# Performance work log

Hardware: AMD Instinct MI355X
Metric: run time of the kernel (lower is better)

## Reference

```python
import jax, jax.numpy as jnp
import numpy as np

N_HEAD = 16


def setup_inputs() -> dict:
    key = jax.random.key(0)
    ks = jax.random.split(key, 5)
    B, L, C = 2, 2048, 1024
    s = 0.02
    return {
        "x": jax.random.normal(ks[0], (B, L, C), dtype=jnp.float32),
        "attn_mask": jnp.ones((B, L), dtype=jnp.int64),
        "Wq": jax.random.normal(ks[1], (C, C), dtype=jnp.float32) * s,
        "Wk": jax.random.normal(ks[2], (C, C), dtype=jnp.float32) * s,
        "Wv": jax.random.normal(ks[3], (C, C), dtype=jnp.float32) * s,
        "Wp": jax.random.normal(ks[4], (C, C), dtype=jnp.float32) * s,
    }


def reference(x, attn_mask, Wq, Wk, Wv, Wp):
    B, L, C = x.shape
    H = N_HEAD
    D = C // H
    # nn.Linear(bias=False): y = x @ W.T with W of shape (out, in)
    q = (x @ Wq.T).reshape(B, L, H, D).transpose(0, 2, 1, 3)  # (B,H,L,D)
    k = (x @ Wk.T).reshape(B, L, H, D).transpose(0, 2, 1, 3)
    v = (x @ Wv.T).reshape(B, L, H, D).transpose(0, 2, 1, 3)
    att = jnp.einsum("bhqd,bhkd->bhqk", q, k) / jnp.sqrt(jnp.asarray(D, x.dtype))
    causal = jnp.tril(jnp.ones((L, L), dtype=bool))  # (L,L)
    tok = (attn_mask != 0)[:, None, None, :]  # (B,1,1,L) key-side padding mask
    mask = causal[None, None, :, :] & tok
    att = jnp.where(mask, att, -jnp.inf)
    att = jax.nn.softmax(att, axis=-1)
    # dropout p=0.0 (eval): identity
    y = jnp.einsum("bhqk,bhkd->bhqd", att, v)
    y = y.transpose(0, 2, 1, 3).reshape(B, L, C)
    return y @ Wp.T
```

## Files before the change

### kernel.cpp

```cpp
#include <hip/hip_runtime.h>
#include <hip/hip_bf16.h>
#include <cstdint>

typedef _Float16 f16;
typedef _Float16 f16x4 __attribute__((ext_vector_type(4)));
typedef _Float16 f16x8 __attribute__((ext_vector_type(8)));
typedef float f32x4 __attribute__((ext_vector_type(4)));

#define LNEG (-1e30f)
#define EXP2(x) __builtin_amdgcn_exp2f(x)

__device__ __forceinline__ f32x4 mfma16(f16x8 a, f16x8 b, f32x4 c){
    return __builtin_amdgcn_mfma_f32_16x16x32_f16(a, b, c, 0, 0, 0);
}

__global__ __launch_bounds__(256) void cvt5(
    const float* __restrict__ x,  const float* __restrict__ wq,
    const float* __restrict__ wk, const float* __restrict__ wv,
    const float* __restrict__ wp, f16* __restrict__ dst, int nx8)
{
    int i = blockIdx.x * blockDim.x + threadIdx.x;
    const float* src; int off;
    if (i < nx8){ src = x; off = i; }
    else {
        int j = i - nx8;
        int s = j >> 17;
        off = j & 131071;
        src = (s == 0) ? wq : (s == 1) ? wk : (s == 2) ? wv : wp;
    }
    const float4* p = (const float4*)src + (size_t)off * 2;
    float4 v0 = p[0], v1 = p[1];
    f16x8 o = { (f16)v0.x, (f16)v0.y, (f16)v0.z, (f16)v0.w,
                (f16)v1.x, (f16)v1.y, (f16)v1.z, (f16)v1.w };
    *(f16x8*)&dst[(size_t)i * 8] = o;
}

template<typename OutT>
__global__ __launch_bounds__(256) void gemm_xwt(
    const f16* __restrict__ A, const f16* __restrict__ W0, size_t wstride,
    OutT* __restrict__ out0, size_t ostride, f16* __restrict__ vtout,
    int M, int N, int K)
{
    const int tid  = threadIdx.x;
    const int lane = tid & 63;
    const int w    = tid >> 6;
    const int wr   = w >> 1, wc = w & 1;
    const int m0   = blockIdx.y * 128;
    const int n0   = blockIdx.x * 128;
    const f16* Wz  = W0 + wstride * blockIdx.z;
    OutT* out      = out0 + ostride * blockIdx.z;

    __shared__ f16 At[2][128 * 64];
    __shared__ f16 Bt[2][128 * 64];

    f32x4 acc[4][4] = {};
    f16x8 avr[4], bvr[4];

    int srow[4], scolb[4], sswz[4];
    #pragma unroll
    for (int j = 0; j < 4; ++j){
        int off  = (j * 256 + tid) * 16;
        srow[j]  = off >> 7;
        scolb[j] = off & 127;
        sswz[j]  = srow[j] * 128 + (scolb[j] ^ ((srow[j] & 7) << 4));
    }

    #pragma unroll
    for (int j = 0; j < 4; ++j){
        avr[j] = *(const f16x8*)&A [(size_t)(m0 + srow[j]) * K + (scolb[j] >> 1)];
        bvr[j] = *(const f16x8*)&Wz[(size_t)(n0 + srow[j]) * K + (scolb[j] >> 1)];
    }
    #pragma unroll
    for (int j = 0; j < 4; ++j){
        *(f16x8*)((char*)At[0] + sswz[j]) = avr[j];
        *(f16x8*)((char*)Bt[0] + sswz[j]) = bvr[j];
    }
    __syncthreads();

    const int NT = K >> 6;
    for (int t = 0; t < NT; ++t){
        const int cur = t & 1;
        const bool pre = (t + 1 < NT);
        if (pre){
            const int k0 = (t + 1) << 6;
            #pragma unroll
            for (int j = 0; j < 4; ++j){
                avr[j] = *(const f16x8*)&A [(size_t)(m0 + srow[j]) * K + k0 + (scolb[j] >> 1)];
                bvr[j] = *(const f16x8*)&Wz[(size_t)(n0 + srow[j]) * K + k0 + (scolb[j] >> 1)];
            }
        }
        #pragma unroll
        for (int kk = 0; kk < 2; ++kk){
            f16x8 af[4], bf[4];
            #pragma unroll
            for (int mf = 0; mf < 4; ++mf){
                int row = wr * 64 + mf * 16 + (lane & 15);
                int cb  = (kk * 64 + 16 * (lane >> 4)) ^ ((row & 7) << 4);
                af[mf] = *(const f16x8*)((const char*)At[cur] + row * 128 + cb);
            }
            #pragma unroll
            for (int nf = 0; nf < 4; ++nf){
                int row = wc * 64 + nf * 16 + (lane & 15);
                int cb  = (kk * 64 + 16 * (lane >> 4)) ^ ((row & 7) << 4);
                bf[nf] = *(const f16x8*)((const char*)Bt[cur] + row * 128 + cb);
            }
            #pragma unroll
            for (int mf = 0; mf < 4; ++mf)
                #pragma unroll
                for (int nf = 0; nf < 4; ++nf)
                    acc[mf][nf] = mfma16(af[mf], bf[nf], acc[mf][nf]);
        }
        if (pre){
            const int nb = cur ^ 1;
            #pragma unroll
            for (int j = 0; j < 4; ++j){
                *(f16x8*)((char*)At[nb] + sswz[j]) = avr[j];
                *(f16x8*)((char*)Bt[nb] + sswz[j]) = bvr[j];
            }
        }
        __syncthreads();
    }

    if (vtout != nullptr && blockIdx.z == 2){
        #pragma unroll
        for (int mf = 0; mf < 4; ++mf)
            #pragma unroll
            for (int nf = 0; nf < 4; ++nf){
                int row = m0 + wr * 64 + mf * 16 + 4 * (lane >> 4);
                int col = n0 + wc * 64 + nf * 16 + (lane & 15);
                int bb = row >> 11, ll = row & 2047;
                int bh = bb * 16 + (col >> 6), dd = col & 63;
                f16x4 o = { (f16)acc[mf][nf][0], (f16)acc[mf][nf][1],
                            (f16)acc[mf][nf][2], (f16)acc[mf][nf][3] };
                *(f16x4*)&vtout[((size_t)(bh * 64 + dd)) * 2048 + ll] = o;
            }
    } else {
        #pragma unroll
        for (int mf = 0; mf < 4; ++mf)
            #pragma unroll
            for (int nf = 0; nf < 4; ++nf)
                #pragma unroll
                for (int r = 0; r < 4; ++r){
                    int row = m0 + wr * 64 + mf * 16 + 4 * (lane >> 4) + r;
                    int col = n0 + wc * 64 + nf * 16 + (lane & 15);
                    out[(size_t)row * N + col] = (OutT)acc[mf][nf][r];
                }
    }
}

__global__ __launch_bounds__(256) void gemm_proj64(
    const f16* __restrict__ A, const f16* __restrict__ W,
    float* __restrict__ out, int M, int N, int K)
{
    const int tid  = threadIdx.x;
    const int lane = tid & 63;
    const int wc   = tid >> 6;
    const int g    = lane >> 4;
    const int qq   = lane & 15;
    const int m0   = blockIdx.y * 64;
    const int n0   = blockIdx.x * 128;

    __shared__ f16 At[2][64 * 64];
    __shared__ f16 Bt[2][128 * 64];

    f32x4 acc[4][2] = {};
    f16x8 avr[2], bvr[4];

    int arow[2], acol[2], aswz[2];
    #pragma unroll
    for (int j = 0; j < 2; ++j){
        int c  = j * 256 + tid;
        arow[j] = c >> 3; acol[j] = (c & 7) * 8;
        aswz[j] = arow[j] * 128 + (((c & 7) * 16) ^ ((arow[j] & 7) << 4));
    }
    int brow[4], bcol[4], bswz[4];
    #pragma unroll
    for (int j = 0; j < 4; ++j){
        int c  = j * 256 + tid;
        brow[j] = c >> 3; bcol[j] = (c & 7) * 8;
        bswz[j] = brow[j] * 128 + (((c & 7) * 16) ^ ((brow[j] & 7) << 4));
    }

    #pragma unroll
    for (int j = 0; j < 2; ++j) avr[j] = *(const f16x8*)&A[(size_t)(m0 + arow[j]) * K + acol[j]];
    #pragma unroll
    for (int j = 0; j < 4; ++j) bvr[j] = *(const f16x8*)&W[(size_t)(n0 + brow[j]) * K + bcol[j]];
    #pragma unroll
    for (int j = 0; j < 2; ++j) *(f16x8*)((char*)At[0] + aswz[j]) = avr[j];
    #pragma unroll
    for (int j = 0; j < 4; ++j) *(f16x8*)((char*)Bt[0] + bswz[j]) = bvr[j];
    __syncthreads();

    const int NT = K >> 6;
    for (int t = 0; t < NT; ++t){
        const int cur = t & 1;
        const bool pre = (t + 1 < NT);
        if (pre){
            const int k0 = (t + 1) << 6;
            #pragma unroll
            for (int j = 0; j < 2; ++j) avr[j] = *(const f16x8*)&A[(size_t)(m0 + arow[j]) * K + k0 + acol[j]];
            #pragma unroll
            for (int j = 0; j < 4; ++j) bvr[j] = *(const f16x8*)&W[(size_t)(n0 + brow[j]) * K + k0 + bcol[j]];
        }
        #pragma unroll
        for (int kk = 0; kk < 2; ++kk){
            f16x8 af[4], bf[2];
            #pragma unroll
            for (int mf = 0; mf < 4; ++mf){
                int row = mf * 16 + qq;
                int cb  = (kk * 64 + 16 * g) ^ ((row & 7) << 4);
                af[mf] = *(const f16x8*)((const char*)At[cur] + row * 128 + cb);
            }
            #pragma unroll
            for (int nf = 0; nf < 2; ++nf){
                int row = wc * 32 + nf * 16 + qq;
                int cb  = (kk * 64 + 16 * g) ^ ((row & 7) << 4);
                bf[nf] = *(const f16x8*)((const char*)Bt[cur] + row * 128 + cb);
            }
            #pragma unroll
            for (int mf = 0; mf < 4; ++mf)
                #pragma unroll
                for (int nf = 0; nf < 2; ++nf)
                    acc[mf][nf] = mfma16(af[mf], bf[nf], acc[mf][nf]);
        }
        if (pre){
            const int nb = cur ^ 1;
            #pragma unroll
            for (int j = 0; j < 2; ++j) *(f16x8*)((char*)At[nb] + aswz[j]) = avr[j];
            #pragma unroll
            for (int j = 0; j < 4; ++j) *(f16x8*)((char*)Bt[nb] + bswz[j]) = bvr[j];
        }
        __syncthreads();
    }
    #pragma unroll
    for (int mf = 0; mf < 4; ++mf)
        #pragma unroll
        for (int nf = 0; nf < 2; ++nf)
            #pragma unroll
            for (int r = 0; r < 4; ++r){
                int row = m0 + mf * 16 + 4 * g + r;
                int col = n0 + wc * 32 + nf * 16 + qq;
                out[(size_t)row * N + col] = acc[mf][nf][r];
            }
}

__global__ __launch_bounds__(256, 4) void attn_fused(
    const f16* __restrict__ q, const f16* __restrict__ k,
    const f16* __restrict__ vt, const int* __restrict__ amask,
    f16* __restrict__ y, float* __restrict__ pO, float* __restrict__ pML)
{
    const int tid  = threadIdx.x;
    const int lane = tid & 63;
    const int w    = tid >> 6;
    const int g    = lane >> 4;
    const int qq   = lane & 15;

    const int lin = blockIdx.x;
    const int bh  = lin & 31;
    const int grp = lin >> 5;
    int qt, ktLo, ktHi, part; bool fin;
    if (grp < 4)      { qt = 19 - grp;  ktLo = 0;  ktHi = qt + 1; fin = true;  part = 0; }
    else if (grp < 16){ qt = 16 + grp;  ktLo = 0;  ktHi = 16;     fin = false; part = 0; }
    else if (grp < 28){ qt = 47 - grp;  ktLo = 16; ktHi = qt + 1; fin = false; part = 1; }
    else              { qt = 43 - grp;  ktLo = 0;  ktHi = qt + 1; fin = true;  part = 0; }

    const int b = bh >> 4, h = bh & 15;
    const int q0w = qt * 64 + w * 16;

    __shared__ char sK[2][64 * 128];
    __shared__ char sV[2][64 * 128];
    __shared__ char sP[4][16 * 128];

    const int srow = (tid * 2) >> 3;
    const int sc8a = (tid * 2) & 7, sc8b = sc8a + 1;
    const int swka = (sc8a * 16) ^ ((srow & 7) << 4);
    const int swkb = (sc8b * 16) ^ ((srow & 7) << 4);
    const f16* kbase  = k  + ((size_t)b * 2048) * 1024 + h * 64;
    const f16* vtbase = vt + (size_t)bh * 64 * 2048;

    const f16 qscale = (f16)(0.125f * 1.44269504088896f);
    f16x8 aq[2];
    #pragma unroll
    for (int f = 0; f < 2; ++f){
        aq[f] = *(const f16x8*)&q[((size_t)(b * 2048 + q0w + qq)) * 1024 + h * 64 + f * 32 + 8 * g];
        #pragma unroll
        for (int j = 0; j < 8; ++j) aq[f][j] *= qscale;
    }

    f32x4 acc_o[4] = {};
    float m_ln = LNEG, l_ln = 0.f;

    char* pbase = sP[w] + qq * 128;
    const int swp = (qq & 7) << 4;

    {
        const int k0p = ktLo * 64;
        f16x8 ka  = *(const f16x8*)(kbase  + (size_t)(k0p + srow) * 1024 + sc8a * 8);
        f16x8 kb2 = *(const f16x8*)(kbase  + (size_t)(k0p + srow) * 1024 + sc8b * 8);
        f16x8 va  = *(const f16x8*)(vtbase + (size_t)srow * 2048 + k0p + sc8a * 8);
        f16x8 vb  = *(const f16x8*)(vtbase + (size_t)srow * 2048 + k0p + sc8b * 8);
        *(f16x8*)(sK[0] + srow * 128 + swka) = ka;
        *(f16x8*)(sK[0] + srow * 128 + swkb) = kb2;
        *(f16x8*)(sV[0] + srow * 128 + swka) = va;
        *(f16x8*)(sV[0] + srow * 128 + swkb) = vb;
    }
    __syncthreads();

    for (int kt = ktLo; kt < ktHi; ++kt){
        const int cur = (kt - ktLo) & 1;
        const int k0 = kt * 64;
        const bool pre = (kt + 1 < ktHi);

        f16x8 ka, kb2, va, vb;
        if (pre){
            const int nk0 = k0 + 64;
            ka  = *(const f16x8*)(kbase  + (size_t)(nk0 + srow) * 1024 + sc8a * 8);
            kb2 = *(const f16x8*)(kbase  + (size_t)(nk0 + srow) * 1024 + sc8b * 8);
            va  = *(const f16x8*)(vtbase + (size_t)srow * 2048 + nk0 + sc8a * 8);
            vb  = *(const f16x8*)(vtbase + (size_t)srow * 2048 + nk0 + sc8b * 8);
        }

        unsigned long long tokbits = __ballot(amask[b * 2048 + k0 + lane] != 0);
        const bool tokall = (tokbits == ~0ull);

        f32x4 acc_s[4] = {};
        #pragma unroll
        for (int kf = 0; kf < 4; ++kf){
            const int keyl = kf * 16 + qq;
            const char* kr = sK[cur] + keyl * 128;
            const int sw = (keyl & 7) << 4;
            #pragma unroll
            for (int f = 0; f < 2; ++f){
                f16x8 ak = *(const f16x8*)(kr + ((f * 64 + 16 * g) ^ sw));
                acc_s[kf] = mfma16(ak, aq[f], acc_s[kf]);
            }
        }

        const bool fullt = (k0 + 63 <= q0w) && tokall;
        float sv[16];
        #pragma unroll
        for (int kf = 0; kf < 4; ++kf)
            #pragma unroll
            for (int r = 0; r < 4; ++r){
                float s = acc_s[kf][r];
                if (!fullt){
                    const int keyl = kf * 16 + 4 * g + r;
                    const bool ok = (k0 + keyl <= q0w + qq) && ((tokbits >> keyl) & 1);
                    s = ok ? s : LNEG;
                }
                sv[kf * 4 + r] = s;
            }

        float tmax = sv[0];
        #pragma unroll
        for (int i = 1; i < 16; ++i) tmax = fmaxf(tmax, sv[i]);
        tmax = fmaxf(tmax, __shfl_xor(tmax, 16));
        tmax = fmaxf(tmax, __shfl_xor(tmax, 32));
        const bool skip = __all(tmax <= m_ln + 8.f);
        float alpha = 1.f;
        if (!skip){
            const float newm = fmaxf(m_ln, tmax);
            alpha = EXP2(m_ln - newm);
            m_ln = newm;
        }
        float rs = 0.f;
        #pragma unroll
        for (int i = 0; i < 16; ++i){ sv[i] = EXP2(sv[i] - m_ln); rs += sv[i]; }
        rs += __shfl_xor(rs, 16);
        rs += __shfl_xor(rs, 32);
        l_ln = l_ln * alpha + rs;
        if (!skip){
            #pragma unroll
            for (int r = 0; r < 4; ++r){
                const float ar = __shfl(alpha, 4 * g + r);
                #pragma unroll
                for (int nf = 0; nf < 4; ++nf) acc_o[nf][r] *= ar;
            }
        }

        #pragma unroll
        for (int kf = 0; kf < 4; ++kf){
            f16x4 pk = { (f16)sv[kf*4+0], (f16)sv[kf*4+1], (f16)sv[kf*4+2], (f16)sv[kf*4+3] };
            *(f16x4*)(pbase + ((kf * 32 + 8 * g) ^ swp)) = pk;
        }
        asm volatile("s_waitcnt lgkmcnt(0)" ::: "memory");
        __builtin_amdgcn_sched_barrier(0);

        #pragma unroll
        for (int f = 0; f < 2; ++f){
            f16x8 ap = *(const f16x8*)(pbase + ((f * 64 + 16 * g) ^ swp));
            #pragma unroll
            for (int nf = 0; nf < 4; ++nf){
                const int d = nf * 16 + qq;
                f16x8 bv = *(const f16x8*)(sV[cur] + d * 128 + ((f * 64 + 16 * g) ^ ((d & 7) << 4)));
                acc_o[nf] = mfma16(ap, bv, acc_o[nf]);
            }
        }

        if (pre){
            const int nb = cur ^ 1;
            *(f16x8*)(sK[nb] + srow * 128 + swka) = ka;
            *(f16x8*)(sK[nb] + srow * 128 + swkb) = kb2;
            *(f16x8*)(sV[nb] + srow * 128 + swka) = va;
            *(f16x8*)(sV[nb] + srow * 128 + swkb) = vb;
        }
        __syncthreads();
    }

    if (fin){
        const float invl = 1.f / l_ln;
        #pragma unroll
        for (int r = 0; r < 4; ++r){
            const float ir = __shfl(invl, 4 * g + r);
            const int row = q0w + 4 * g + r;
            #pragma unroll
            for (int nf = 0; nf < 4; ++nf)
                y[((size_t)(b * 2048 + row)) * 1024 + h * 64 + nf * 16 + qq] = (f16)(acc_o[nf][r] * ir);
        }
    } else {
        const int qi = qt - 20;
        const size_t base = (((size_t)part * 12 + qi) * 32 + bh) * 64;
        #pragma unroll
        for (int r = 0; r < 4; ++r){
            const int row_local = w * 16 + 4 * g + r;
            float* po = pO + (base + row_local) * 64;
            #pragma unroll
            for (int nf = 0; nf < 4; ++nf)
                po[nf * 16 + qq] = acc_o[nf][r];
        }
        if (lane < 16){
            const size_t mlb = (base + w * 16 + lane) * 2;
            pML[mlb]     = m_ln;
            pML[mlb + 1] = l_ln;
        }
    }
}

__global__ __launch_bounds__(256) void attn_merge(
    const float* __restrict__ pO, const float* __restrict__ pML, f16* __restrict__ y)
{
    const int t = blockIdx.x * 256 + threadIdx.x;
    const int dc = (t & 3) * 16;
    const int rowg = t >> 2;
    const int row = rowg & 63;
    const int bh  = (rowg >> 6) & 31;
    const int qi  = rowg >> 11;
    const size_t rbase = ((size_t)qi * 32 + bh) * 64 + row;
    const size_t PST = (size_t)12 * 32 * 64;

    const float mA = pML[rbase * 2],         lA = pML[rbase * 2 + 1];
    const float mB = pML[(PST + rbase) * 2], lB = pML[(PST + rbase) * 2 + 1];
    const float m  = fmaxf(mA, mB);
    const float wA = EXP2(mA - m), wB = EXP2(mB - m);
    const float inv = 1.f / (wA * lA + wB * lB);

    const float4* oA = (const float4*)(pO + rbase * 64 + dc);
    const float4* oB = (const float4*)(pO + (PST * 64) + rbase * 64 + dc);
    float ov[16];
    #pragma unroll
    for (int j = 0; j < 4; ++j){
        float4 a = oA[j], bb4 = oB[j];
        ov[j*4+0] = (wA * a.x + wB * bb4.x) * inv;
        ov[j*4+1] = (wA * a.y + wB * bb4.y) * inv;
        ov[j*4+2] = (wA * a.z + wB * bb4.z) * inv;
        ov[j*4+3] = (wA * a.w + wB * bb4.w) * inv;
    }
    const int b = bh >> 4, h = bh & 15;
    const int grow = (20 + qi) * 64 + row;
    f16* yp = &y[((size_t)(b * 2048 + grow)) * 1024 + h * 64 + dc];
    f16x8 o0 = { (f16)ov[0],(f16)ov[1],(f16)ov[2],(f16)ov[3],(f16)ov[4],(f16)ov[5],(f16)ov[6],(f16)ov[7] };
    f16x8 o1 = { (f16)ov[8],(f16)ov[9],(f16)ov[10],(f16)ov[11],(f16)ov[12],(f16)ov[13],(f16)ov[14],(f16)ov[15] };
    *(f16x8*)yp = o0;
    *(f16x8*)(yp + 8) = o1;
}

extern "C" void kernel_launch(void* const* d_in, const int* in_sizes, int n_in,
                              void* d_out, int out_size, void* d_ws, size_t ws_size,
                              hipStream_t stream){
    const float* x  = (const float*)d_in[0];
    const int*   am = (const int*)d_in[1];
    const float* Wq = (const float*)d_in[2];
    const float* Wk = (const float*)d_in[3];
    const float* Wv = (const float*)d_in[4];
    const float* Wp = (const float*)d_in[5];
    float* out = (float*)d_out;

    char* ws = (char*)d_ws;
    const size_t XE = (size_t)4096 * 1024;
    const size_t WE = (size_t)1024 * 1024;

    f16* x16 = (f16*)(ws);
    f16* w16 = (f16*)(ws + XE * 2);
    f16* qkv = (f16*)(ws + XE * 2 + WE * 8);
    f16* vt  = (f16*)(ws + XE * 2 + WE * 8 + XE * 6);
    f16* y16 = (f16*)(ws + XE * 2 + WE * 8 + XE * 8);
    float* pO  = (float*)ws;
    float* pML = (float*)(ws + (size_t)2*12*32*64*64*4);

    cvt5<<<4096, 256, 0, stream>>>(x, Wq, Wk, Wv, Wp, x16, (int)(XE / 8));

    gemm_xwt<f16><<<dim3(8, 32, 3), 256, 0, stream>>>(x16, w16, WE, qkv, XE, vt, 4096, 1024, 1024);

    attn_fused<<<dim3(1408), 256, 0, stream>>>(qkv, qkv + XE, vt, am, y16, pO, pML);

    attn_merge<<<384, 256, 0, stream>>>(pO, pML, y16);

    gemm_proj64<<<dim3(8, 64), 256, 0, stream>>>(y16, w16 + 3 * WE, out, 4096, 1024, 1024);
}
```

Baseline: 108.6 us.

## Rebalance attention work split, single-buffer K/V LDS for higher occupancy, fp16 partials

```diff
diff --git a/kernel.cpp b/kernel.cpp
--- a/kernel.cpp
+++ b/kernel.cpp
@@ -244,10 +244,25 @@
             }
 }
 
-__global__ __launch_bounds__(256, 4) void attn_fused(
+#define JE(qt,lo,hi,fin,part) ((uint32_t)((qt)|((lo)<<5)|((hi)<<11)|((fin)<<17)|((part)<<18)))
+__constant__ uint32_t JMAP[48] = {
+    JE(15,0,16,1,0), JE(31,0,16,0,0), JE(31,16,32,0,1), JE(30,0,16,0,0),
+    JE(14,0,15,1,0), JE(30,16,31,0,1), JE(29,0,15,0,0), JE(29,15,30,0,1), JE(28,0,15,0,0),
+    JE(13,0,14,1,0), JE(28,15,29,0,1), JE(27,0,14,0,0), JE(27,14,28,0,1), JE(26,0,14,0,0),
+    JE(12,0,13,1,0), JE(26,14,27,0,1), JE(25,0,13,0,0), JE(25,13,26,0,1), JE(24,0,13,0,0),
+    JE(11,0,12,1,0), JE(24,13,25,0,1), JE(23,0,12,0,0), JE(23,12,24,0,1), JE(22,0,12,0,0),
+    JE(10,0,11,1,0), JE(22,12,23,0,1), JE(21,0,11,0,0), JE(21,11,22,0,1), JE(20,0,11,0,0),
+    JE(9,0,10,1,0),  JE(20,11,21,0,1), JE(19,0,10,0,0), JE(19,10,20,0,1), JE(18,0,10,0,0),
+    JE(8,0,9,1,0),   JE(18,10,19,0,1), JE(17,0,9,0,0),  JE(17,9,18,0,1),  JE(16,0,9,0,0),
+    JE(7,0,8,1,0),   JE(16,9,17,0,1),
+    JE(6,0,7,1,0), JE(5,0,6,1,0), JE(4,0,5,1,0), JE(3,0,4,1,0), JE(2,0,3,1,0),
+    JE(1,0,2,1,0), JE(0,0,1,1,0)
+};
+
+__global__ __launch_bounds__(256, 6) void attn_fused(
     const f16* __restrict__ q, const f16* __restrict__ k,
     const f16* __restrict__ vt, const int* __restrict__ amask,
-    f16* __restrict__ y, float* __restrict__ pO, float* __restrict__ pML)
+    f16* __restrict__ y, f16* __restrict__ pOh, float* __restrict__ pML)
 {
     const int tid  = threadIdx.x;
     const int lane = tid & 63;
@@ -257,18 +272,18 @@
 
     const int lin = blockIdx.x;
     const int bh  = lin & 31;
-    const int grp = lin >> 5;
-    int qt, ktLo, ktHi, part; bool fin;
-    if (grp < 4)      { qt = 19 - grp;  ktLo = 0;  ktHi = qt + 1; fin = true;  part = 0; }
-    else if (grp < 16){ qt = 16 + grp;  ktLo = 0;  ktHi = 16;     fin = false; part = 0; }
-    else if (grp < 28){ qt = 47 - grp;  ktLo = 16; ktHi = qt + 1; fin = false; part = 1; }
-    else              { qt = 43 - grp;  ktLo = 0;  ktHi = qt + 1; fin = true;  part = 0; }
+    const uint32_t je = JMAP[lin >> 5];
+    const int qt   = je & 31;
+    const int ktLo = (je >> 5) & 63;
+    const int ktHi = (je >> 11) & 63;
+    const bool fin = (je >> 17) & 1;
+    const int part = (je >> 18) & 1;
 
     const int b = bh >> 4, h = bh & 15;
     const int q0w = qt * 64 + w * 16;
 
-    __shared__ char sK[2][64 * 128];
-    __shared__ char sV[2][64 * 128];
+    __shared__ char sK[64 * 128];
+    __shared__ char sV[64 * 128];
     __shared__ char sP[4][16 * 128];
 
     const int srow = (tid * 2) >> 3;
@@ -299,15 +314,14 @@
         f16x8 kb2 = *(const f16x8*)(kbase  + (size_t)(k0p + srow) * 1024 + sc8b * 8);
         f16x8 va  = *(const f16x8*)(vtbase + (size_t)srow * 2048 + k0p + sc8a * 8);
         f16x8 vb  = *(const f16x8*)(vtbase + (size_t)srow * 2048 + k0p + sc8b * 8);
-        *(f16x8*)(sK[0] + srow * 128 + swka) = ka;
-        *(f16x8*)(sK[0] + srow * 128 + swkb) = kb2;
-        *(f16x8*)(sV[0] + srow * 128 + swka) = va;
-        *(f16x8*)(sV[0] + srow * 128 + swkb) = vb;
+        *(f16x8*)(sK + srow * 128 + swka) = ka;
+        *(f16x8*)(sK + srow * 128 + swkb) = kb2;
+        *(f16x8*)(sV + srow * 128 + swka) = va;
+        *(f16x8*)(sV + srow * 128 + swkb) = vb;
     }
     __syncthreads();
 
     for (int kt = ktLo; kt < ktHi; ++kt){
-        const int cur = (kt - ktLo) & 1;
         const int k0 = kt * 64;
         const bool pre = (kt + 1 < ktHi);
 
@@ -327,7 +341,7 @@
         #pragma unroll
         for (int kf = 0; kf < 4; ++kf){
             const int keyl = kf * 16 + qq;
-            const char* kr = sK[cur] + keyl * 128;
+            const char* kr = sK + keyl * 128;
             const int sw = (keyl & 7) << 4;
             #pragma unroll
             for (int f = 0; f < 2; ++f){
@@ -392,19 +406,19 @@
             #pragma unroll
             for (int nf = 0; nf < 4; ++nf){
                 const int d = nf * 16 + qq;
-                f16x8 bv = *(const f16x8*)(sV[cur] + d * 128 + ((f * 64 + 16 * g) ^ ((d & 7) << 4)));
+                f16x8 bv = *(const f16x8*)(sV + d * 128 + ((f * 64 + 16 * g) ^ ((d & 7) << 4)));
                 acc_o[nf] = mfma16(ap, bv, acc_o[nf]);
             }
         }
 
         if (pre){
-            const int nb = cur ^ 1;
-            *(f16x8*)(sK[nb] + srow * 128 + swka) = ka;
-            *(f16x8*)(sK[nb] + srow * 128 + swkb) = kb2;
-            *(f16x8*)(sV[nb] + srow * 128 + swka) = va;
-            *(f16x8*)(sV[nb] + srow * 128 + swkb) = vb;
-        }
-        __syncthreads();
+            __syncthreads();
+            *(f16x8*)(sK + srow * 128 + swka) = ka;
+            *(f16x8*)(sK + srow * 128 + swkb) = kb2;
+            *(f16x8*)(sV + srow * 128 + swka) = va;
+            *(f16x8*)(sV + srow * 128 + swkb) = vb;
+            __syncthreads();
+        }
     }
 
     if (fin){
@@ -418,15 +432,15 @@
                 y[((size_t)(b * 2048 + row)) * 1024 + h * 64 + nf * 16 + qq] = (f16)(acc_o[nf][r] * ir);
         }
     } else {
-        const int qi = qt - 20;
-        const size_t base = (((size_t)part * 12 + qi) * 32 + bh) * 64;
+        const int slot = ((qt - 16) << 1) | part;
+        const size_t base = ((size_t)slot * 32 + bh) * 64;
         #pragma unroll
         for (int r = 0; r < 4; ++r){
             const int row_local = w * 16 + 4 * g + r;
-            float* po = pO + (base + row_local) * 64;
+            f16* po = pOh + (base + row_local) * 64;
             #pragma unroll
             for (int nf = 0; nf < 4; ++nf)
-                po[nf * 16 + qq] = acc_o[nf][r];
+                po[nf * 16 + qq] = (f16)acc_o[nf][r];
         }
         if (lane < 16){
             const size_t mlb = (base + w * 16 + lane) * 2;
@@ -437,7 +451,7 @@
 }
 
 __global__ __launch_bounds__(256) void attn_merge(
-    const float* __restrict__ pO, const float* __restrict__ pML, f16* __restrict__ y)
+    const f16* __restrict__ pOh, const float* __restrict__ pML, f16* __restrict__ y)
 {
     const int t = blockIdx.x * 256 + threadIdx.x;
     const int dc = (t & 3) * 16;
@@ -445,31 +459,27 @@
     const int row = rowg & 63;
     const int bh  = (rowg >> 6) & 31;
     const int qi  = rowg >> 11;
-    const size_t rbase = ((size_t)qi * 32 + bh) * 64 + row;
-    const size_t PST = (size_t)12 * 32 * 64;
-
-    const float mA = pML[rbase * 2],         lA = pML[rbase * 2 + 1];
-    const float mB = pML[(PST + rbase) * 2], lB = pML[(PST + rbase) * 2 + 1];
+    const size_t rbA = ((size_t)(qi * 2)     * 32 + bh) * 64 + row;
+    const size_t rbB = ((size_t)(qi * 2 + 1) * 32 + bh) * 64 + row;
+
+    const float mA = pML[rbA * 2], lA = pML[rbA * 2 + 1];
+    const float mB = pML[rbB * 2], lB = pML[rbB * 2 + 1];
     const float m  = fmaxf(mA, mB);
     const float wA = EXP2(mA - m), wB = EXP2(mB - m);
     const float inv = 1.f / (wA * lA + wB * lB);
 
-    const float4* oA = (const float4*)(pO + rbase * 64 + dc);
-    const float4* oB = (const float4*)(pO + (PST * 64) + rbase * 64 + dc);
-    float ov[16];
-    #pragma unroll
-    for (int j = 0; j < 4; ++j){
-        float4 a = oA[j], bb4 = oB[j];
-        ov[j*4+0] = (wA * a.x + wB * bb4.x) * inv;
-        ov[j*4+1] = (wA * a.y + wB * bb4.y) * inv;
-        ov[j*4+2] = (wA * a.z + wB * bb4.z) * inv;
-        ov[j*4+3] = (wA * a.w + wB * bb4.w) * inv;
+    const f16x8* oA = (const f16x8*)(pOh + rbA * 64 + dc);
+    const f16x8* oB = (const f16x8*)(pOh + rbB * 64 + dc);
+    f16x8 a0 = oA[0], a1 = oA[1], b0 = oB[0], b1 = oB[1];
+    f16x8 o0, o1;
+    #pragma unroll
+    for (int j = 0; j < 8; ++j){
+        o0[j] = (f16)((wA * (float)a0[j] + wB * (float)b0[j]) * inv);
+        o1[j] = (f16)((wA * (float)a1[j] + wB * (float)b1[j]) * inv);
     }
     const int b = bh >> 4, h = bh & 15;
-    const int grow = (20 + qi) * 64 + row;
+    const int grow = (16 + qi) * 64 + row;
     f16* yp = &y[((size_t)(b * 2048 + grow)) * 1024 + h * 64 + dc];
-    f16x8 o0 = { (f16)ov[0],(f16)ov[1],(f16)ov[2],(f16)ov[3],(f16)ov[4],(f16)ov[5],(f16)ov[6],(f16)ov[7] };
-    f16x8 o1 = { (f16)ov[8],(f16)ov[9],(f16)ov[10],(f16)ov[11],(f16)ov[12],(f16)ov[13],(f16)ov[14],(f16)ov[15] };
     *(f16x8*)yp = o0;
     *(f16x8*)(yp + 8) = o1;
 }
@@ -494,16 +504,16 @@
     f16* qkv = (f16*)(ws + XE * 2 + WE * 8);
     f16* vt  = (f16*)(ws + XE * 2 + WE * 8 + XE * 6);
     f16* y16 = (f16*)(ws + XE * 2 + WE * 8 + XE * 8);
-    float* pO  = (float*)ws;
-    float* pML = (float*)(ws + (size_t)2*12*32*64*64*4);
+    f16*   pOh = (f16*)ws;
+    float* pML = (float*)(ws + (size_t)32 * 32 * 64 * 64 * 2);
 
     cvt5<<<4096, 256, 0, stream>>>(x, Wq, Wk, Wv, Wp, x16, (int)(XE / 8));
 
     gemm_xwt<f16><<<dim3(8, 32, 3), 256, 0, stream>>>(x16, w16, WE, qkv, XE, vt, 4096, 1024, 1024);
 
-    attn_fused<<<dim3(1408), 256, 0, stream>>>(qkv, qkv + XE, vt, am, y16, pO, pML);
-
-    attn_merge<<<384, 256, 0, stream>>>(pO, pML, y16);
+    attn_fused<<<dim3(1536), 256, 0, stream>>>(qkv, qkv + XE, vt, am, y16, pOh, pML);
+
+    attn_merge<<<512, 256, 0, stream>>>(pOh, pML, y16);
 
     gemm_proj64<<<dim3(8, 64), 256, 0, stream>>>(y16, w16 + 3 * WE, out, 4096, 1024, 1024);
 }
```

Measured after the change: 142.0 us. +30.8%, slower.
